# Optimization experiments

Measured on AMD Instinct MI355X. Metric: run time of the kernel, lower is better.

The kernel has to match this reference:

```python
import jax, jax.numpy as jnp
import numpy as np

T = 2048            # flattened tokens (vLLM style)
D = 4096            # hidden_size
NSSM = 128          # ssm_state_size
K = 4               # conv kernel size
G = 8               # n_groups
H = 128             # mamba_num_heads
P = 64              # mamba_head_dim
INTER = H * P       # 8192 = expand * hidden_size
CONV_DIM = INTER + 2 * G * NSSM   # 10240 (x, B, C share the conv)
PROJ = INTER + CONV_DIM + H       # 18560 (z, xBC, dt)
Q = 128             # SSD chunk size
EPS = 1e-5


def setup_inputs() -> dict:
    key = jax.random.key(0)
    ks = jax.random.split(key, 9)
    s = 0.02
    return {
        "hidden_states": jax.random.normal(ks[0], (T, D), jnp.float32),
        "residual": jax.random.normal(ks[1], (T, D), jnp.float32),
        "norm_w": jnp.ones((D,), jnp.float32),
        "in_proj_w": jax.random.normal(ks[2], (PROJ, D), jnp.float32) * s,
        "conv_w": jax.random.normal(ks[3], (CONV_DIM, K), jnp.float32) * 0.2,
        "conv_b": jax.random.normal(ks[4], (CONV_DIM,), jnp.float32) * 0.1,
        "A_log": jnp.log(jax.random.uniform(ks[5], (H,), jnp.float32, 1.0, 16.0)),
        "D_res": jax.random.normal(ks[6], (H,), jnp.float32) * 0.5 + 1.0,
        "dt_bias": jax.random.normal(ks[7], (H,), jnp.float32) * 0.5,
        "gn_w": jnp.ones((INTER,), jnp.float32),
        "out_proj_w": jax.random.normal(ks[8], (D, INTER), jnp.float32) * s,
    }


def _forward(hidden_states, residual, norm_w, in_proj_w, conv_w, conv_b,
             A_log, D_res, dt_bias, gn_w, out_proj_w):
    # ---- fused add + RMSNorm (vLLM RMSNorm(hidden, residual)) ----
    resid = hidden_states + residual
    hs = resid * jax.lax.rsqrt(jnp.mean(resid * resid, -1, keepdims=True) + EPS) * norm_w

    # ---- MambaMixer2 ----
    proj = hs @ in_proj_w.T                              # [T, PROJ]
    z, xBC, dt = jnp.split(proj, [INTER, INTER + CONV_DIM], axis=-1)

    # causal depthwise conv1d over time + SiLU
    xp = jnp.pad(xBC, ((K - 1, 0), (0, 0)))
    conv = conv_b + sum(conv_w[:, k] * xp[k:k + T] for k in range(K))
    xBC = jax.nn.silu(conv)

    x, B, C = jnp.split(xBC, [INTER, INTER + G * NSSM], axis=-1)
    x = x.reshape(T, H, P)
    Bh = jnp.repeat(B.reshape(T, G, NSSM), H // G, axis=1)   # [T,H,N]
    Ch = jnp.repeat(C.reshape(T, G, NSSM), H // G, axis=1)   # [T,H,N]

    dt = jax.nn.softplus(dt + dt_bias)                   # [T,H]
    A = -jnp.exp(A_log)                                  # [H] (negative)

    # ---- SSD chunked selective scan ----
    NC = T // Q
    a = (dt * A).reshape(NC, Q, H)                       # per-step log decay (<=0)
    cum = jnp.cumsum(a, axis=1)                          # inclusive cumsum, [NC,Q,H]
    Xd = (dt[:, :, None] * x).reshape(NC, Q, H, P)
    Bc = Bh.reshape(NC, Q, H, NSSM)
    Cc = Ch.reshape(NC, Q, H, NSSM)

    # intra-chunk: Y[i] = sum_{j<=i} (C_i.B_j) exp(cum_i-cum_j) Xd_j
    CB = jnp.einsum('cqhn,ckhn->chqk', Cc, Bc)
    cumT = cum.transpose(0, 2, 1)                        # [NC,H,Q]
    mask = jnp.tril(jnp.ones((Q, Q), bool))
    Lm = jnp.where(mask, jnp.exp(cumT[:, :, :, None] - cumT[:, :, None, :]), 0.0)
    Y = jnp.einsum('chqk,ckhp->cqhp', CB * Lm, Xd)

    # chunk-local end states, then scan states across chunks
    cum_end = cum[:, -1]                                 # [NC,H]
    decay_out = jnp.exp(cum_end[:, None] - cum)          # [NC,Q,H]
    S_loc = jnp.einsum('cqhn,cqh,cqhp->chnp', Bc, decay_out, Xd)
    chunk_decay = jnp.exp(cum_end)                       # [NC,H]

    def step(s, inp):
        dec, sl = inp
        return dec[:, None, None] * s + sl, s            # emit state BEFORE chunk

    _, S_prev = jax.lax.scan(step, jnp.zeros((H, NSSM, P), x.dtype),
                             (chunk_decay, S_loc))       # [NC,H,N,P]

    # inter-chunk contribution + skip connection D*x
    Y = Y + jnp.einsum('cqhn,cqh,chnp->cqhp', Cc, jnp.exp(cum), S_prev)
    y = Y.reshape(T, H, P) + D_res[None, :, None] * x

    # gated RMSNorm then out projection
    y = y.reshape(T, INTER) * jax.nn.silu(z)
    y = y * jax.lax.rsqrt(jnp.mean(y * y, -1, keepdims=True) + EPS) * gn_w
    return y @ out_proj_w.T, resid


def reference(hidden_states, residual, norm_w, in_proj_w, conv_w, conv_b,
              A_log, D_res, dt_bias, gn_w, out_proj_w):
    return _forward(hidden_states, residual, norm_w, in_proj_w, conv_w, conv_b,
                    A_log, D_res, dt_bias, gn_w, out_proj_w)
```

## Files before the change

### kernel.cpp

```cpp
#include <hip/hip_runtime.h>
#include <stdint.h>

typedef unsigned short u16;
typedef unsigned int   u32;
typedef float  f32x4  __attribute__((ext_vector_type(4)));
typedef __bf16 bf16x8 __attribute__((ext_vector_type(8)));
typedef u16    u16x4  __attribute__((ext_vector_type(4)));
typedef u16    u16x8  __attribute__((ext_vector_type(8)));

#define T_N     2048
#define D_N     4096
#define H_N     128
#define P_N     64
#define G_N     8
#define NS_N    128
#define INTER_N 8192
#define CONVD_N 10240
#define PROJ_N  18560
#define NGEMM_N 18432
#define NC_N    16

__device__ __forceinline__ float bf2f(u16 u){ u32 x = ((u32)u) << 16; return __builtin_bit_cast(float, x); }
__device__ __forceinline__ u16 f2bf(float f){
  u32 u = __builtin_bit_cast(u32, f);
  u += 0x7FFFu + ((u >> 16) & 1u);
  return (u16)(u >> 16);
}

__device__ __forceinline__ void gld_lds16(const void* g, void* lds){
  __builtin_amdgcn_global_load_lds(
      (const __attribute__((address_space(1))) void*)(uintptr_t)g,
      (__attribute__((address_space(3))) void*)(u32)(uintptr_t)lds,
      16, 0, 0);
}

__global__ __launch_bounds__(256)
void k_addnorm(const float* __restrict__ hin, const float* __restrict__ rin,
               const float* __restrict__ nw, float* __restrict__ resid,
               u16* __restrict__ hs16, float* __restrict__ rstd){
  __shared__ float red[4];
  const int row = blockIdx.x, tid = threadIdx.x;
  const size_t rb = (size_t)row * D_N;
  f32x4 s[4];
  float ss = 0.f;
  #pragma unroll
  for (int i = 0; i < 4; ++i){
    int c4 = tid + i*256;
    f32x4 a = *(const f32x4*)&hin[rb + (size_t)c4*4];
    f32x4 b = *(const f32x4*)&rin[rb + (size_t)c4*4];
    s[i] = a + b;
    *(f32x4*)&resid[rb + (size_t)c4*4] = s[i];
    ss += s[i][0]*s[i][0] + s[i][1]*s[i][1] + s[i][2]*s[i][2] + s[i][3]*s[i][3];
  }
  #pragma unroll
  for (int o = 32; o > 0; o >>= 1) ss += __shfl_down(ss, o, 64);
  if ((tid & 63) == 0) red[tid >> 6] = ss;
  __syncthreads();
  float tot = (red[0] + red[1]) + (red[2] + red[3]);
  float rs = rsqrtf(tot / (float)D_N + 1e-5f);
  if (tid == 0) rstd[row] = rs;
  #pragma unroll
  for (int i = 0; i < 4; ++i){
    int c4 = tid + i*256;
    f32x4 w = *(const f32x4*)&nw[(size_t)c4*4];
    u16x4 o = { f2bf(s[i][0]*rs*w[0]), f2bf(s[i][1]*rs*w[1]),
                f2bf(s[i][2]*rs*w[2]), f2bf(s[i][3]*rs*w[3]) };
    *(u16x4*)&hs16[rb + (size_t)c4*4] = o;
  }
}

__global__ void k_cvt(const float* __restrict__ in, u16* __restrict__ out, size_t n4){
  size_t i = (size_t)blockIdx.x * blockDim.x + threadIdx.x;
  size_t stride = (size_t)gridDim.x * blockDim.x;
  for (; i < n4; i += stride){
    f32x4 v = *(const f32x4*)&in[i*4];
    u16x4 o = { f2bf(v[0]), f2bf(v[1]), f2bf(v[2]), f2bf(v[3]) };
    *(u16x4*)&out[i*4] = o;
  }
}

__global__ void k_wdt(const float* __restrict__ W, const float* __restrict__ nw,
                      float* __restrict__ Wn){
  int idx = blockIdx.x*256 + threadIdx.x;
  int d = idx >> 7, h = idx & 127;
  Wn[(size_t)d*128 + h] = W[(size_t)(INTER_N + CONVD_N + h)*D_N + d] * nw[d];
}

__global__ __launch_bounds__(256)
void k_dtgemm(const float* __restrict__ resid, const float* __restrict__ Wn,
              float* __restrict__ dtpart){
  __shared__ float lhs[16*128];
  const int tid = threadIdx.x;
  const int tb = blockIdx.x >> 3, ks = blockIdx.x & 7;
  const int t0 = tb * 16;
  const int k0 = ks * (D_N / 8);
  const int hcol = tid & 127, rh = tid >> 7;
  float acc[8] = {0,0,0,0,0,0,0,0};
  for (int kt = k0; kt < k0 + D_N/8; kt += 128){
    __syncthreads();
    #pragma unroll
    for (int it = 0; it < 2; ++it){
      int idx = it*256 + tid;
      int rr = idx >> 5, c4 = idx & 31;
      *(f32x4*)&lhs[rr*128 + c4*4] = *(const f32x4*)&resid[(size_t)(t0+rr)*D_N + kt + c4*4];
    }
    __syncthreads();
    #pragma unroll 4
    for (int kk4 = 0; kk4 < 32; ++kk4){
      f32x4 w4;
      #pragma unroll
      for (int j = 0; j < 4; ++j) w4[j] = Wn[(size_t)(kt + kk4*4 + j)*128 + hcol];
      #pragma unroll
      for (int j = 0; j < 8; ++j){
        f32x4 lv = *(const f32x4*)&lhs[(rh*8 + j)*128 + kk4*4];
        acc[j] += lv[0]*w4[0] + lv[1]*w4[1] + lv[2]*w4[2] + lv[3]*w4[3];
      }
    }
  }
  #pragma unroll
  for (int j = 0; j < 8; ++j){
    int t = t0 + rh*8 + j;
    dtpart[((size_t)ks*T_N + t)*128 + hcol] = acc[j];
  }
}

__global__ void k_dtprep(const float* __restrict__ dtpart, const float* __restrict__ rstd,
                         const float* __restrict__ dt_bias, const float* __restrict__ A_log,
                         float* __restrict__ dtv, float* __restrict__ cum,
                         float* __restrict__ cumend, float* __restrict__ dec){
  int c = blockIdx.x, h = threadIdx.x;
  float A = -expf(A_log[h]);
  float bias = dt_bias[h];
  float cm = 0.f;
  for (int q = 0; q < 128; ++q){
    int t = c*128 + q;
    float s = 0.f;
    #pragma unroll
    for (int kspl = 0; kspl < 8; ++kspl)
      s += dtpart[((size_t)kspl*T_N + t)*128 + h];
    float x = s * rstd[t] + bias;
    float dv = (x > 20.f) ? x : log1pf(expf(x));
    dtv[(size_t)t*128 + h] = dv;
    cm += dv * A;
    cum[(size_t)t*128 + h] = cm;
  }
  cumend[c*128 + h] = cm;
  dec[c*128 + h] = expf(cm);
}

#define STA(BUF,HH,KT) gld_lds16(pA + (size_t)((HH)*64)*K + (size_t)(KT)*64, shb + (BUF)*BSZ + (HH)*8192 + tid*16)
#define STB(BUF,HH,KT) gld_lds16(pB[HH] + (size_t)(KT)*64, shb + (BUF)*BSZ + 32768 + (HH)*8192 + tid*16)
#define VMWN do { asm volatile("s_waitcnt vmcnt(%0)" :: "n"(NFRAG) : "memory"); __builtin_amdgcn_sched_barrier(0); } while(0)
#define PH_RD(BUF, Q)                                                                   \
    bf16x8 aa00 = *(const bf16x8*)(shb + (BUF)*BSZ + rdA + (Q)*4096 + sA0);             \
    bf16x8 aa01 = *(const bf16x8*)(shb + (BUF)*BSZ + rdA + (Q)*4096 + sA1);             \
    bf16x8 aa10 = *(const bf16x8*)(shb + (BUF)*BSZ + rdA + (Q)*4096 + 2048 + sA0);      \
    bf16x8 aa11 = *(const bf16x8*)(shb + (BUF)*BSZ + rdA + (Q)*4096 + 2048 + sA1);
#define PH_RB(BUF, BB)                                                                  \
    _Pragma("unroll") for (int nn = 0; nn < NFRAG; ++nn){                               \
      BB[nn][0] = *(const bf16x8*)(shb + (BUF)*BSZ + rdB + nn*2048 + sA0);              \
      BB[nn][1] = *(const bf16x8*)(shb + (BUF)*BSZ + rdB + nn*2048 + sA1);              \
    }
#define PH_MM(Q, BB)                                                                    \
    __builtin_amdgcn_s_setprio(1);                                                      \
    _Pragma("unroll") for (int nn = 0; nn < NFRAG; ++nn){                               \
      acc[(Q)*2+0][nn] = __builtin_amdgcn_mfma_f32_16x16x32_bf16(aa00, BB[nn][0], acc[(Q)*2+0][nn],0,0,0); \
      acc[(Q)*2+0][nn] = __builtin_amdgcn_mfma_f32_16x16x32_bf16(aa01, BB[nn][1], acc[(Q)*2+0][nn],0,0,0); \
      acc[(Q)*2+1][nn] = __builtin_amdgcn_mfma_f32_16x16x32_bf16(aa10, BB[nn][0], acc[(Q)*2+1][nn],0,0,0); \
      acc[(Q)*2+1][nn] = __builtin_amdgcn_mfma_f32_16x16x32_bf16(aa11, BB[nn][1], acc[(Q)*2+1][nn],0,0,0); \
    }                                                                                   \
    __builtin_amdgcn_s_setprio(0);                                                      \
    __builtin_amdgcn_s_barrier();                                                       \
    __builtin_amdgcn_sched_barrier(0);

template<int NFRAG, typename OT>
__global__ __launch_bounds__(512, 2)
void k_gemm256(const u16* __restrict__ A, const u16* __restrict__ Bm,
               OT* __restrict__ C, int ldc, int K, int nkt, size_t zstride){
  constexpr int BSZ = 32768 + NFRAG*8192;
  __shared__ char shb[2*BSZ];
  const int tid = threadIdx.x, ln = tid & 63, wid = tid >> 6;
  const int wm = wid >> 2, wn = wid & 3;
  const int lr = ln & 15, lg = ln >> 4;

  const int gx = gridDim.x;
  const int nwg = gx * gridDim.y;
  const int lin = blockIdx.y * gx + blockIdx.x;
  const int qq = nwg >> 3;
  const int swz = (lin & 7)*qq + (lin >> 3);
  const int m0 = (swz / gx) << 8;
  const int n0 = (swz % gx) * (NFRAG*64);
  const int kbase = blockIdx.z * nkt;

  const int srow = tid >> 3;
  const int slog = ((tid & 7) ^ (srow & 7)) * 8;
  const u16* pA = A + (size_t)(m0 + srow)*K + (size_t)kbase*64 + slog;
  const u16* pB[NFRAG];
  #pragma unroll
  for (int hh = 0; hh < NFRAG; ++hh)
    pB[hh] = Bm + (size_t)(n0 + hh*64 + srow)*K + (size_t)kbase*64 + slog;

  const int sA0 = (lg ^ (ln & 7)) << 4;
  const int sA1 = ((4 + lg) ^ (ln & 7)) << 4;
  const u32 rdA = wm*16384 + lr*128;
  const u32 rdB = 32768 + (wn*NFRAG*16 + lr)*128;

  f32x4 acc[8][NFRAG] = {};

  #pragma unroll
  for (int hh = 0; hh < 4; ++hh) STA(0, hh, 0);
  #pragma unroll
  for (int hh = 0; hh < NFRAG; ++hh) STB(0, hh, 0);
  #pragma unroll
  for (int hh = 0; hh < NFRAG; ++hh) STB(1, hh, 1);
  VMWN;
  __builtin_amdgcn_s_barrier();
  __builtin_amdgcn_sched_barrier(0);

  const int nit = nkt >> 1;
  #pragma unroll 1
  for (int it = 0; it < nit; ++it){
    const int t1 = 2*it + 1;
    int t2 = 2*it + 2; if (t2 >= nkt) t2 = 0;
    int t3 = 2*it + 3; if (t3 >= nkt) t3 = 1;
    bf16x8 bb0[NFRAG][2], bb1[NFRAG][2];
    { PH_RD(0,0) PH_RB(0, bb0)
      #pragma unroll
      for (int hh = 0; hh < 4; ++hh) STA(1, hh, t1);
      PH_MM(0, bb0) }
    { PH_RD(0,1)
      #pragma unroll
      for (int hh = 0; hh < NFRAG; ++hh) STB(0, hh, t2);
      PH_MM(1, bb0) }
    { PH_RD(0,2)
      PH_MM(2, bb0) }
    { PH_RD(0,3)
      VMWN;
      PH_MM(3, bb0) }
    { PH_RD(1,0) PH_RB(1, bb1)
      #pragma unroll
      for (int hh = 0; hh < 4; ++hh) STA(0, hh, t2);
      PH_MM(0, bb1) }
    { PH_RD(1,1)
      #pragma unroll
      for (int hh = 0; hh < NFRAG; ++hh) STB(1, hh, t3);
      PH_MM(1, bb1) }
    { PH_RD(1,2)
      PH_MM(2, bb1) }
    { PH_RD(1,3)
      VMWN;
      PH_MM(3, bb1) }
  }
  asm volatile("s_waitcnt vmcnt(0)" ::: "memory");

  OT* Cz = C + (size_t)blockIdx.z * zstride;
  const int crow = m0 + wm*128 + lg*4;
  const int ccol = n0 + wn*(NFRAG*16) + lr;
  #pragma unroll
  for (int m = 0; m < 8; ++m)
    #pragma unroll
    for (int nn = 0; nn < NFRAG; ++nn)
      #pragma unroll
      for (int r = 0; r < 4; ++r){
        float v = acc[m][nn][r];
        if constexpr (__is_same(OT, float))
          Cz[(size_t)(crow + m*16 + r)*ldc + ccol + nn*16] = v;
        else
          Cz[(size_t)(crow + m*16 + r)*ldc + ccol + nn*16] = f2bf(v);
      }
}

__global__ __launch_bounds__(256)
void k_add2(const float* __restrict__ a, const float* __restrict__ b,
            float* __restrict__ o, int n4){
  int i = blockIdx.x*256 + threadIdx.x;
  if (i < n4){
    f32x4 x = *(const f32x4*)&a[(size_t)i*4];
    f32x4 y = *(const f32x4*)&b[(size_t)i*4];
    x = x + y;
    *(f32x4*)&o[(size_t)i*4] = x;
  }
}

__global__ __launch_bounds__(256)
void k_conv(const u16* __restrict__ proj16, const float* __restrict__ cw,
            const float* __restrict__ cb, u16* __restrict__ x16,
            u16* __restrict__ B16, u16* __restrict__ C16){
  const int ch = blockIdx.x*256 + threadIdx.x;
  const int tbase = blockIdx.y*64;
  f32x4 w = *(const f32x4*)&cw[(size_t)ch*4];
  const float bias = cb[ch];
  const u16* pcol = proj16 + INTER_N + ch;
  float p0 = 0.f, p1 = 0.f, p2 = 0.f;
  if (tbase >= 3){
    p0 = bf2f(pcol[(size_t)(tbase-3)*PROJ_N]);
    p1 = bf2f(pcol[(size_t)(tbase-2)*PROJ_N]);
    p2 = bf2f(pcol[(size_t)(tbase-1)*PROJ_N]);
  }
  u16* xdst = (ch < INTER_N) ? x16 + ch
            : (ch < INTER_N + 1024) ? B16 + (ch - INTER_N)
            : C16 + (ch - INTER_N - 1024);
  const int dstride = (ch < INTER_N) ? INTER_N : 1024;
  #pragma unroll 4
  for (int i = 0; i < 64; ++i){
    int t = tbase + i;
    float cur = bf2f(pcol[(size_t)t*PROJ_N]);
    float acc = bias + w[0]*p0 + w[1]*p1 + w[2]*p2 + w[3]*cur;
    float v = acc / (1.f + __expf(-acc));
    xdst[(size_t)t*dstride] = f2bf(v);
    p0 = p1; p1 = p2; p2 = cur;
  }
}

__global__ __launch_bounds__(512)
void k_ssda(const u16* __restrict__ B16, const u16* __restrict__ x16,
            const float* __restrict__ dtv, const float* __restrict__ cum,
            const float* __restrict__ cumend, u16* __restrict__ SlocT){
  __shared__ u16 lBdT[128*136];
  __shared__ u16 lXdT[64*136];
  __shared__ float lDec[128], lDt[128];
  const int tid = threadIdx.x, wid = tid >> 6, ln = tid & 63;
  const int c = blockIdx.x >> 7, h = blockIdx.x & 127, g = h >> 4;
  if (tid < 128){
    int t = c*128 + tid;
    lDec[tid] = __expf(cumend[c*128 + h] - cum[(size_t)t*128 + h]);
    lDt[tid]  = dtv[(size_t)t*128 + h];
  }
  __syncthreads();
  for (int it = 0; it < 32; ++it){
    int idx = it*512 + tid;
    int q = idx >> 7, n = idx & 127;
    float bv = bf2f(B16[(size_t)(c*128 + q)*1024 + g*128 + n]) * lDec[q];
    lBdT[n*136 + q] = f2bf(bv);
  }
  for (int it = 0; it < 16; ++it){
    int idx = it*512 + tid;
    int q = idx >> 6, p = idx & 63;
    float xv = bf2f(x16[(size_t)(c*128 + q)*INTER_N + h*64 + p]) * lDt[q];
    lXdT[p*136 + q] = f2bf(xv);
  }
  __syncthreads();
  const int wr = wid >> 1, wc = wid & 1;
  const int kofs = (ln >> 4) << 3;
  f32x4 acc[2][2] = {};
  #pragma unroll
  for (int ks = 0; ks < 4; ++ks){
    bf16x8 a[2], b[2];
    #pragma unroll
    for (int m = 0; m < 2; ++m) a[m] = *(const bf16x8*)&lBdT[(wr*32 + m*16 + (ln & 15))*136 + ks*32 + kofs];
    #pragma unroll
    for (int n = 0; n < 2; ++n) b[n] = *(const bf16x8*)&lXdT[(wc*32 + n*16 + (ln & 15))*136 + ks*32 + kofs];
    #pragma unroll
    for (int m = 0; m < 2; ++m)
      #pragma unroll
      for (int n = 0; n < 2; ++n)
        acc[m][n] = __builtin_amdgcn_mfma_f32_16x16x32_bf16(a[m], b[n], acc[m][n], 0, 0, 0);
  }
  const size_t base = (size_t)(c*128 + h) * 8192;
  #pragma unroll
  for (int m = 0; m < 2; ++m)
    #pragma unroll
    for (int n = 0; n < 2; ++n){
      int p  = wc*32 + n*16 + (ln & 15);
      int nn = wr*32 + m*16 + ((ln >> 4) << 2);
      u16x4 o = { f2bf(acc[m][n][0]), f2bf(acc[m][n][1]), f2bf(acc[m][n][2]), f2bf(acc[m][n][3]) };
      *(u16x4*)&SlocT[base + (size_t)p*128 + nn] = o;
    }
}

__global__ __launch_bounds__(256)
void k_scan(const u16* __restrict__ SlocT, const float* __restrict__ dec,
            u16* __restrict__ SprevT){
  int idx = blockIdx.x*256 + threadIdx.x;
  int h = idx >> 11, p = (idx >> 5) & 63, n4 = idx & 31;
  float s0 = 0.f, s1 = 0.f, s2 = 0.f, s3 = 0.f;
  for (int c = 0; c < NC_N; ++c){
    size_t off = (size_t)(c*128 + h)*8192 + (size_t)p*128 + n4*4;
    u16x4 o = { f2bf(s0), f2bf(s1), f2bf(s2), f2bf(s3) };
    *(u16x4*)&SprevT[off] = o;
    u16x4 sl = *(const u16x4*)&SlocT[off];
    float d = dec[c*128 + h];
    s0 = d*s0 + bf2f(sl[0]); s1 = d*s1 + bf2f(sl[1]);
    s2 = d*s2 + bf2f(sl[2]); s3 = d*s3 + bf2f(sl[3]);
  }
}

__global__ __launch_bounds__(512)
void k_ssdb(const u16* __restrict__ C16, const u16* __restrict__ B16g,
            const u16* __restrict__ x16, const float* __restrict__ dtv,
            const float* __restrict__ cum, const u16* __restrict__ SprevT,
            const u16* __restrict__ proj16, const float* __restrict__ Dres,
            u16* __restrict__ yg16){
  __shared__ u16 lC[128*136];
  __shared__ u16 lBP[128*136];
  __shared__ u16 lXdT[64*136];
  __shared__ float lCum[128], lDt[128];
  const int tid = threadIdx.x, wid = tid >> 6, ln = tid & 63;
  const int c = blockIdx.x >> 7, h = blockIdx.x & 127, g = h >> 4;
  if (tid < 128){
    int t = c*128 + tid;
    lCum[tid] = cum[(size_t)t*128 + h];
    lDt[tid]  = dtv[(size_t)t*128 + h];
  }
  __syncthreads();
  for (int it = 0; it < 32; ++it){
    int idx = it*512 + tid;
    int q = idx >> 7, n = idx & 127;
    size_t gi = (size_t)(c*128 + q)*1024 + g*128 + n;
    lC[q*136 + n]  = C16[gi];
    lBP[q*136 + n] = B16g[gi];
  }
  for (int it = 0; it < 16; ++it){
    int idx = it*512 + tid;
    int q = idx >> 6, p = idx & 63;
    lXdT[p*136 + q] = f2bf(bf2f(x16[(size_t)(c*128 + q)*INTER_N + h*64 + p]) * lDt[q]);
  }
  __syncthreads();
  const int kofs = (ln >> 4) << 3;
  {
    const int wr = wid >> 2, wc = wid & 3;
    f32x4 cb[4][2] = {};
    #pragma unroll
    for (int ks = 0; ks < 4; ++ks){
      bf16x8 a[4], b[2];
      #pragma unroll
      for (int m = 0; m < 4; ++m) a[m] = *(const bf16x8*)&lC[(wr*64 + m*16 + (ln & 15))*136 + ks*32 + kofs];
      #pragma unroll
      for (int n = 0; n < 2; ++n) b[n] = *(const bf16x8*)&lBP[(wc*32 + n*16 + (ln & 15))*136 + ks*32 + kofs];
      #pragma unroll
      for (int m = 0; m < 4; ++m)
        #pragma unroll
        for (int n = 0; n < 2; ++n)
          cb[m][n] = __builtin_amdgcn_mfma_f32_16x16x32_bf16(a[m], b[n], cb[m][n], 0, 0, 0);
    }
    __syncthreads();
    #pragma unroll
    for (int m = 0; m < 4; ++m)
      #pragma unroll
      for (int n = 0; n < 2; ++n){
        int kcol = (wid & 3)*32 + n*16 + (ln & 15);
        float ck = lCum[kcol];
        #pragma unroll
        for (int r = 0; r < 4; ++r){
          int q = (wid >> 2)*64 + m*16 + ((ln >> 4) << 2) + r;
          float v = (kcol <= q) ? cb[m][n][r] * __expf(lCum[q] - ck) : 0.f;
          lBP[q*136 + kcol] = f2bf(v);
        }
      }
  }
  __syncthreads();
  const int yr = wid >> 1, yc = wid & 1;
  f32x4 y1[2][2] = {}, y2[2][2] = {};
  const size_t spbase = (size_t)(c*128 + h) * 8192;
  #pragma unroll
  for (int ks = 0; ks < 4; ++ks){
    bf16x8 ap[2], acf[2], bx[2], bs[2];
    #pragma unroll
    for (int m = 0; m < 2; ++m){
      int qr = yr*32 + m*16 + (ln & 15);
      ap[m]  = *(const bf16x8*)&lBP[qr*136 + ks*32 + kofs];
      acf[m] = *(const bf16x8*)&lC [qr*136 + ks*32 + kofs];
    }
    #pragma unroll
    for (int n = 0; n < 2; ++n){
      int p = yc*32 + n*16 + (ln & 15);
      bx[n] = *(const bf16x8*)&lXdT[p*136 + ks*32 + kofs];
      bs[n] = *(const bf16x8*)&SprevT[spbase + (size_t)p*128 + ks*32 + kofs];
    }
    #pragma unroll
    for (int m = 0; m < 2; ++m)
      #pragma unroll
      for (int n = 0; n < 2; ++n){
        y1[m][n] = __builtin_amdgcn_mfma_f32_16x16x32_bf16(ap[m],  bx[n], y1[m][n], 0, 0, 0);
        y2[m][n] = __builtin_amdgcn_mfma_f32_16x16x32_bf16(acf[m], bs[n], y2[m][n], 0, 0, 0);
      }
  }
  const float dh = Dres[h];
  #pragma unroll
  for (int m = 0; m < 2; ++m)
    #pragma unroll
    for (int r = 0; r < 4; ++r){
      int q = yr*32 + m*16 + ((ln >> 4) << 2) + r;
      float eq = __expf(lCum[q]);
      size_t t = (size_t)(c*128 + q);
      #pragma unroll
      for (int n = 0; n < 2; ++n){
        int p = yc*32 + n*16 + (ln & 15);
        int chn = h*64 + p;
        float xv = bf2f(x16[t*INTER_N + chn]);
        float zv = bf2f(proj16[t*PROJ_N + chn]);
        float yv = y1[m][n][r] + eq*y2[m][n][r] + dh*xv;
        float sg = zv / (1.f + __expf(-zv));
        yg16[t*INTER_N + chn] = f2bf(yv * sg);
      }
    }
}

__global__ __launch_bounds__(256)
void k_gnorm(const u16* __restrict__ yg, const float* __restrict__ gnw,
             u16* __restrict__ yn16){
  __shared__ float red[4];
  const int row = blockIdx.x, tid = threadIdx.x;
  const u16* rp = yg + (size_t)row * INTER_N;
  u16x8 v[4];
  float ss = 0.f;
  #pragma unroll
  for (int i = 0; i < 4; ++i){
    v[i] = *(const u16x8*)&rp[(size_t)(tid + i*256)*8];
    #pragma unroll
    for (int j = 0; j < 8; ++j){ float f = bf2f(v[i][j]); ss += f*f; }
  }
  #pragma unroll
  for (int o = 32; o > 0; o >>= 1) ss += __shfl_down(ss, o, 64);
  if ((tid & 63) == 0) red[tid >> 6] = ss;
  __syncthreads();
  float tot = (red[0] + red[1]) + (red[2] + red[3]);
  float sc = rsqrtf(tot / (float)INTER_N + 1e-5f);
  #pragma unroll
  for (int i = 0; i < 4; ++i){
    int c8 = (tid + i*256)*8;
    u16x8 o;
    #pragma unroll
    for (int j = 0; j < 8; ++j)
      o[j] = f2bf(bf2f(v[i][j]) * sc * gnw[c8 + j]);
    *(u16x8*)&yn16[(size_t)row*INTER_N + c8] = o;
  }
}

extern "C" void kernel_launch(void* const* d_in, const int* in_sizes, int n_in,
                              void* d_out, int out_size, void* d_ws, size_t ws_size,
                              hipStream_t stream){
  (void)in_sizes; (void)n_in; (void)out_size;
  const float* hs_in     = (const float*)d_in[0];
  const float* res_in    = (const float*)d_in[1];
  const float* norm_w    = (const float*)d_in[2];
  const float* in_proj_w = (const float*)d_in[3];
  const float* conv_w    = (const float*)d_in[4];
  const float* conv_b    = (const float*)d_in[5];
  const float* A_log     = (const float*)d_in[6];
  const float* D_res     = (const float*)d_in[7];
  const float* dt_bias   = (const float*)d_in[8];
  const float* gn_w      = (const float*)d_in[9];
  const float* out_proj_w= (const float*)d_in[10];

  float* out0      = (float*)d_out;
  float* resid_out = out0 + (size_t)T_N * D_N;

  char* ws = (char*)d_ws;
  const size_t o_hs16   = 0;
  const size_t o_Win16  = 16777216;
  const size_t o_Wout16 = 168820736;
  const size_t o_proj   = 235929600;
  const size_t o_plane  = 311951360;
  const size_t o_Wn     = 387973120;
  const size_t o_dtv    = 391118848;
  const size_t o_cum    = 392167424;
  const size_t o_cumend = 393216000;
  const size_t o_dec    = 393224192;
  const size_t o_rstd   = 393232384;
  const size_t o_x16    = 393240576;
  const size_t o_B16    = 426795008;
  const size_t o_C16    = 430989312;
  const size_t o_SlocT  = 435183616;
  const size_t o_SprevT = 468738048;
  const size_t o_yn16   = 502292480;
  const size_t WS_NEED  = 535846912;
  if (ws_size < WS_NEED) return;

  u16*   hs16   = (u16*)  (ws + o_hs16);
  u16*   Win16  = (u16*)  (ws + o_Win16);
  u16*   Wout16 = (u16*)  (ws + o_Wout16);
  u16*   proj16 = (u16*)  (ws + o_proj);
  float* planes = (float*)(ws + o_plane);
  float* Wn     = (float*)(ws + o_Wn);
  float* dtpart = (float*)(ws + o_proj);
  float* dtv    = (float*)(ws + o_dtv);
  float* cum    = (float*)(ws + o_cum);
  float* cumend = (float*)(ws + o_cumend);
  float* dec    = (float*)(ws + o_dec);
  float* rstd   = (float*)(ws + o_rstd);
  u16*   x16    = (u16*)  (ws + o_x16);
  u16*   B16    = (u16*)  (ws + o_B16);
  u16*   C16    = (u16*)  (ws + o_C16);
  u16*   SlocT  = (u16*)  (ws + o_SlocT);
  u16*   SprevT = (u16*)  (ws + o_SprevT);
  u16*   yn16   = (u16*)  (ws + o_yn16);
  u16*   yg16   = (u16*)  (ws + o_Win16);

  k_addnorm<<<T_N, 256, 0, stream>>>(hs_in, res_in, norm_w, resid_out, hs16, rstd);
  k_cvt<<<4096, 256, 0, stream>>>(in_proj_w,  Win16,  (size_t)NGEMM_N * D_N / 4);
  k_cvt<<<2048, 256, 0, stream>>>(out_proj_w, Wout16, (size_t)D_N * INTER_N / 4);
  k_wdt<<<2048, 256, 0, stream>>>(in_proj_w, norm_w, Wn);
  k_dtgemm<<<1024, 256, 0, stream>>>(resid_out, Wn, dtpart);
  k_dtprep<<<NC_N, 128, 0, stream>>>(dtpart, rstd, dt_bias, A_log, dtv, cum, cumend, dec);
  k_gemm256<3, u16><<<dim3(NGEMM_N/192, T_N/256, 1), 512, 0, stream>>>(hs16, Win16, proj16, PROJ_N, D_N, D_N/64, 0);
  k_conv<<<dim3(CONVD_N/256, T_N/64), 256, 0, stream>>>(proj16, conv_w, conv_b, x16, B16, C16);
  k_ssda<<<NC_N * H_N, 512, 0, stream>>>(B16, x16, dtv, cum, cumend, SlocT);
  k_scan<<<1024, 256, 0, stream>>>(SlocT, dec, SprevT);
  k_ssdb<<<NC_N * H_N, 512, 0, stream>>>(C16, B16, x16, dtv, cum, SprevT, proj16, D_res, yg16);
  k_gnorm<<<T_N, 256, 0, stream>>>(yg16, gn_w, yn16);
  k_gemm256<4, float><<<dim3(D_N/256, T_N/256, 2), 512, 0, stream>>>(yn16, Wout16, planes, D_N, INTER_N, INTER_N/64/2, (size_t)T_N*D_N);
  k_add2<<<T_N*D_N/1024, 256, 0, stream>>>(planes, planes + (size_t)T_N*D_N, out0, T_N*D_N/4);
}
```

Baseline: 948.6 us.

## Merge GEMM phases into fewer barriers and remap tiles per XCD

The GEMM main loop now reads two A sub-fragments per phase and issues two MFMA groups before each barrier, which halves the barriers per k-tile from eight to four. The workgroup-to-tile mapping also changes so each XCD owns a contiguous band of N columns, iterating over M inside it, with the aim of improving L2 reuse of the B (weight) tiles. The cost is more live A registers per phase, which could add register pressure at 2 waves/SIMD. The VMWN waits now sit in the merged phases, so global loads have less room to overlap with compute. The new mapping assumes gridDim.x is a multiple of 8.

New measurement: 952.6 us. Within noise of the previous version (+0.4%).

```diff
diff --git a/kernel.cpp b/kernel.cpp
--- a/kernel.cpp
+++ b/kernel.cpp
@@ -151,24 +151,24 @@
 #define STA(BUF,HH,KT) gld_lds16(pA + (size_t)((HH)*64)*K + (size_t)(KT)*64, shb + (BUF)*BSZ + (HH)*8192 + tid*16)
 #define STB(BUF,HH,KT) gld_lds16(pB[HH] + (size_t)(KT)*64, shb + (BUF)*BSZ + 32768 + (HH)*8192 + tid*16)
 #define VMWN do { asm volatile("s_waitcnt vmcnt(%0)" :: "n"(NFRAG) : "memory"); __builtin_amdgcn_sched_barrier(0); } while(0)
-#define PH_RD(BUF, Q)                                                                   \
-    bf16x8 aa00 = *(const bf16x8*)(shb + (BUF)*BSZ + rdA + (Q)*4096 + sA0);             \
-    bf16x8 aa01 = *(const bf16x8*)(shb + (BUF)*BSZ + rdA + (Q)*4096 + sA1);             \
-    bf16x8 aa10 = *(const bf16x8*)(shb + (BUF)*BSZ + rdA + (Q)*4096 + 2048 + sA0);      \
-    bf16x8 aa11 = *(const bf16x8*)(shb + (BUF)*BSZ + rdA + (Q)*4096 + 2048 + sA1);
-#define PH_RB(BUF, BB)                                                                  \
+#define RDA(BUF, Q, V0, V1, V2, V3)                                                     \
+    bf16x8 V0 = *(const bf16x8*)(shb + (BUF)*BSZ + rdA + (Q)*4096 + sA0);               \
+    bf16x8 V1 = *(const bf16x8*)(shb + (BUF)*BSZ + rdA + (Q)*4096 + sA1);               \
+    bf16x8 V2 = *(const bf16x8*)(shb + (BUF)*BSZ + rdA + (Q)*4096 + 2048 + sA0);        \
+    bf16x8 V3 = *(const bf16x8*)(shb + (BUF)*BSZ + rdA + (Q)*4096 + 2048 + sA1);
+#define RDB(BUF, BB)                                                                    \
     _Pragma("unroll") for (int nn = 0; nn < NFRAG; ++nn){                               \
       BB[nn][0] = *(const bf16x8*)(shb + (BUF)*BSZ + rdB + nn*2048 + sA0);              \
       BB[nn][1] = *(const bf16x8*)(shb + (BUF)*BSZ + rdB + nn*2048 + sA1);              \
     }
-#define PH_MM(Q, BB)                                                                    \
-    __builtin_amdgcn_s_setprio(1);                                                      \
+#define MM8(Q, V0, V1, V2, V3, BB)                                                      \
     _Pragma("unroll") for (int nn = 0; nn < NFRAG; ++nn){                               \
-      acc[(Q)*2+0][nn] = __builtin_amdgcn_mfma_f32_16x16x32_bf16(aa00, BB[nn][0], acc[(Q)*2+0][nn],0,0,0); \
-      acc[(Q)*2+0][nn] = __builtin_amdgcn_mfma_f32_16x16x32_bf16(aa01, BB[nn][1], acc[(Q)*2+0][nn],0,0,0); \
-      acc[(Q)*2+1][nn] = __builtin_amdgcn_mfma_f32_16x16x32_bf16(aa10, BB[nn][0], acc[(Q)*2+1][nn],0,0,0); \
-      acc[(Q)*2+1][nn] = __builtin_amdgcn_mfma_f32_16x16x32_bf16(aa11, BB[nn][1], acc[(Q)*2+1][nn],0,0,0); \
-    }                                                                                   \
+      acc[(Q)*2+0][nn] = __builtin_amdgcn_mfma_f32_16x16x32_bf16(V0, BB[nn][0], acc[(Q)*2+0][nn],0,0,0); \
+      acc[(Q)*2+0][nn] = __builtin_amdgcn_mfma_f32_16x16x32_bf16(V1, BB[nn][1], acc[(Q)*2+0][nn],0,0,0); \
+      acc[(Q)*2+1][nn] = __builtin_amdgcn_mfma_f32_16x16x32_bf16(V2, BB[nn][0], acc[(Q)*2+1][nn],0,0,0); \
+      acc[(Q)*2+1][nn] = __builtin_amdgcn_mfma_f32_16x16x32_bf16(V3, BB[nn][1], acc[(Q)*2+1][nn],0,0,0); \
+    }
+#define ENDPH                                                                           \
     __builtin_amdgcn_s_setprio(0);                                                      \
     __builtin_amdgcn_s_barrier();                                                       \
     __builtin_amdgcn_sched_barrier(0);
@@ -184,12 +184,11 @@
   const int lr = ln & 15, lg = ln >> 4;
 
   const int gx = gridDim.x;
-  const int nwg = gx * gridDim.y;
   const int lin = blockIdx.y * gx + blockIdx.x;
-  const int qq = nwg >> 3;
-  const int swz = (lin & 7)*qq + (lin >> 3);
-  const int m0 = (swz / gx) << 8;
-  const int n0 = (swz % gx) * (NFRAG*64);
+  const int xcd = lin & 7, sub = lin >> 3;
+  const int ncx = gx >> 3;
+  const int m0 = (sub / ncx) << 8;
+  const int n0 = (xcd * ncx + (sub % ncx)) * (NFRAG*64);
   const int kbase = blockIdx.z * nkt;
 
   const int srow = tid >> 3;
@@ -224,32 +223,44 @@
     int t2 = 2*it + 2; if (t2 >= nkt) t2 = 0;
     int t3 = 2*it + 3; if (t3 >= nkt) t3 = 1;
     bf16x8 bb0[NFRAG][2], bb1[NFRAG][2];
-    { PH_RD(0,0) PH_RB(0, bb0)
+    {
+      RDA(0,0, x0,x1,x2,x3) RDA(0,1, y0,y1,y2,y3) RDB(0, bb0)
       #pragma unroll
       for (int hh = 0; hh < 4; ++hh) STA(1, hh, t1);
-      PH_MM(0, bb0) }
-    { PH_RD(0,1)
+      __builtin_amdgcn_s_setprio(1);
+      MM8(0, x0,x1,x2,x3, bb0)
+      MM8(1, y0,y1,y2,y3, bb0)
+      ENDPH
+    }
+    {
+      RDA(0,2, x0,x1,x2,x3) RDA(0,3, y0,y1,y2,y3)
       #pragma unroll
       for (int hh = 0; hh < NFRAG; ++hh) STB(0, hh, t2);
-      PH_MM(1, bb0) }
-    { PH_RD(0,2)
-      PH_MM(2, bb0) }
-    { PH_RD(0,3)
       VMWN;
-      PH_MM(3, bb0) }
-    { PH_RD(1,0) PH_RB(1, bb1)
+      __builtin_amdgcn_s_setprio(1);
+      MM8(2, x0,x1,x2,x3, bb0)
+      MM8(3, y0,y1,y2,y3, bb0)
+      ENDPH
+    }
+    {
+      RDA(1,0, x0,x1,x2,x3) RDA(1,1, y0,y1,y2,y3) RDB(1, bb1)
       #pragma unroll
       for (int hh = 0; hh < 4; ++hh) STA(0, hh, t2);
-      PH_MM(0, bb1) }
-    { PH_RD(1,1)
+      __builtin_amdgcn_s_setprio(1);
+      MM8(0, x0,x1,x2,x3, bb1)
+      MM8(1, y0,y1,y2,y3, bb1)
+      ENDPH
+    }
+    {
+      RDA(1,2, x0,x1,x2,x3) RDA(1,3, y0,y1,y2,y3)
       #pragma unroll
       for (int hh = 0; hh < NFRAG; ++hh) STB(1, hh, t3);
-      PH_MM(1, bb1) }
-    { PH_RD(1,2)
-      PH_MM(2, bb1) }
-    { PH_RD(1,3)
       VMWN;
-      PH_MM(3, bb1) }
+      __builtin_amdgcn_s_setprio(1);
+      MM8(2, x0,x1,x2,x3, bb1)
+      MM8(3, y0,y1,y2,y3, bb1)
+      ENDPH
+    }
   }
   asm volatile("s_waitcnt vmcnt(0)" ::: "memory");
 
```
